# Performance work log

Measured on AMD Instinct MI355X. Metric: run time of the kernel, lower is better.

## Reference

```python
import jax, jax.numpy as jnp
import numpy as np

B, L, D_IN, D_GATE, D_HID, D_STATE = 4, 8192, 512, 2048, 128, 512
EPS = 1e-5


def _layernorm(x, g, b):
    m = jnp.mean(x, axis=-1, keepdims=True)
    v = jnp.var(x, axis=-1, keepdims=True)
    return (x - m) * jax.lax.rsqrt(v + EPS) * g + b


def _dss(u, g, b, lam_re, lam_im, c_re, c_im, d):
    # u: [B, L, H]; diagonal state-space mixing along L via FFT conv
    seq_len = u.shape[-2]
    un = _layernorm(u, g, b)
    residual = un * d                                   # learned skip, [B,L,H]
    lam = -jnp.exp(lam_re) + 1j * jnp.exp(lam_im)       # [N] complex
    c = (c_re + 1j * c_im) * (jnp.exp(lam) - 1.0) / lam  # [H,N]
    t = jnp.arange(seq_len, dtype=jnp.float32)
    s = jnp.exp(t[:, None] * lam[None, :])              # [L,N] Vandermonde
    kern = jnp.einsum('hn,ln->lh', c, s).real           # [L,H]
    n_fft = 2 * seq_len
    uf = jnp.fft.rfft(un, n=n_fft, axis=-2)             # [B, n_fft/2+1, H]
    kf = jnp.fft.rfft(kern, n=n_fft, axis=0)            # [n_fft/2+1, H]
    y = jnp.fft.irfft(uf * kf, n=n_fft, axis=-2)[..., :seq_len, :]
    return y + residual


def setup_inputs() -> dict:
    key = jax.random.key(0)
    ks = jax.random.split(key, 16)
    f32 = jnp.float32
    return {
        'x': jax.random.normal(ks[0], (B, L, D_IN), f32),
        'norm_g': jnp.ones((D_IN,), f32),
        'norm_b': jnp.zeros((D_IN,), f32),
        'W_v': jax.random.normal(ks[1], (D_GATE, D_IN), f32) / np.sqrt(D_IN),
        'W_u': jax.random.normal(ks[2], (D_HID, D_IN), f32) / np.sqrt(D_IN),
        'W_uc': jax.random.normal(ks[3], (D_GATE, D_HID), f32) / np.sqrt(D_HID),
        'W_o': jax.random.normal(ks[4], (D_IN, D_GATE), f32) / np.sqrt(D_GATE),
        'b_o': jnp.zeros((D_IN,), f32),
        'dss_g': jnp.ones((D_HID,), f32),
        'dss_b': jnp.zeros((D_HID,), f32),
        'lam_re': jax.random.normal(ks[5], (D_STATE,), f32),
        'lam_im': jax.random.normal(ks[6], (D_STATE,), f32),
        'C_re': jax.random.normal(ks[7], (D_HID, D_STATE), f32) / np.sqrt(D_STATE),
        'C_im': jax.random.normal(ks[8], (D_HID, D_STATE), f32) / np.sqrt(D_STATE),
        'D_skip': jax.random.normal(ks[9], (D_HID,), f32),
    }


def reference(x, norm_g, norm_b, W_v, W_u, W_uc, W_o, b_o,
              dss_g, dss_b, lam_re, lam_im, C_re, C_im, D_skip):
    xn = _layernorm(x, norm_g, norm_b)
    v = jax.nn.gelu(jnp.einsum('blf,gf->blg', xn, W_v), approximate=False)  # [B,L,G]
    u = jax.nn.gelu(jnp.einsum('blf,hf->blh', xn, W_u), approximate=False)  # [B,L,H]
    y = _dss(u, dss_g, dss_b, lam_re, lam_im, C_re, C_im, D_skip)           # [B,L,H]
    uc = jnp.einsum('blh,gh->blg', y, W_uc)                                 # [B,L,G]
    o = jnp.einsum('blg,fg->blf', uc * v, W_o) + b_o                        # [B,L,F]
    return o + x
```

## Files before the change

kernel.cpp:

```cpp
#include <hip/hip_runtime.h>
#include <math.h>
#include <stdint.h>

typedef unsigned short u16;
typedef unsigned int   u32;
typedef short short8 __attribute__((ext_vector_type(8)));
typedef float v4f    __attribute__((ext_vector_type(4)));

#define DEVI static __device__ __forceinline__

struct __align__(8)  U2 { u32 x, y; };
struct __align__(16) U4 { u32 x, y, z, w; };

static const int BB = 4, LL = 8192;
static const int BL = BB * LL;

DEVI float bf2f(u16 u){ u32 v = ((u32)u) << 16; float f; __builtin_memcpy(&f, &v, 4); return f; }
DEVI u16  f2bf(float f){ u32 u; __builtin_memcpy(&u, &f, 4); return (u16)((u + 0x7fffu + ((u >> 16) & 1u)) >> 16); }

DEVI float geluf(float x){
  float z = fabsf(x) * 0.7071067811865475f;
  float t = __builtin_amdgcn_rcpf(1.0f + 0.3275911f * z);
  float p = t * (0.254829592f + t * (-0.284496736f + t * (1.421413741f +
            t * (-1.453152027f + t * 1.061405429f))));
  float e = __builtin_amdgcn_exp2f(z * z * -1.4426950408889634f);
  float er = 1.0f - p * e;
  float s = (x < 0.0f) ? -er : er;
  return 0.5f * x * (1.0f + s);
}

DEVI void ldsload16(const void* g, void* l){
  __builtin_amdgcn_global_load_lds(
      (const __attribute__((address_space(1))) u32*)(uintptr_t)g,
      (__attribute__((address_space(3)))  u32*)(u32)(uintptr_t)l,
      16, 0, 0);
}

__global__ __launch_bounds__(256) void k_cvt4(
    const float* __restrict__ s0, u16* __restrict__ d0, int n0,
    const float* __restrict__ s1, u16* __restrict__ d1, int n1,
    const float* __restrict__ s2, u16* __restrict__ d2, int n2,
    const float* __restrict__ s3, u16* __restrict__ d3, int n3){
  int i = blockIdx.x * 256 + threadIdx.x;
  if (i < n0){ d0[i] = f2bf(s0[i]); return; }
  i -= n0;
  if (i < n1){ d1[i] = f2bf(s1[i]); return; }
  i -= n1;
  if (i < n2){ d2[i] = f2bf(s2[i]); return; }
  i -= n2;
  if (i < n3){ d3[i] = f2bf(s3[i]); }
}

__global__ __launch_bounds__(256) void k_ln1(const float* __restrict__ x, const float* __restrict__ g,
                                             const float* __restrict__ b, u16* __restrict__ xn){
  int row = blockIdx.x, t = threadIdx.x;
  const float2* xr = (const float2*)(x + (int64_t)row * 512);
  float2 p = xr[t];
  float s = p.x + p.y, ss = p.x * p.x + p.y * p.y;
  for (int off = 32; off; off >>= 1){ s += __shfl_down(s, off); ss += __shfl_down(ss, off); }
  __shared__ float red[8];
  int w = t >> 6, lane = t & 63;
  if (!lane){ red[w] = s; red[4 + w] = ss; }
  __syncthreads();
  s  = red[0] + red[1] + red[2] + red[3];
  ss = red[4] + red[5] + red[6] + red[7];
  float m = s * (1.0f / 512.0f), var = ss * (1.0f / 512.0f) - m * m;
  float rs = rsqrtf(var + 1e-5f);
  float2 gv = ((const float2*)g)[t], bv = ((const float2*)b)[t];
  float r0 = (p.x - m) * rs * gv.x + bv.x;
  float r1 = (p.y - m) * rs * gv.y + bv.y;
  ((u32*)(xn + (int64_t)row * 512))[t] = (u32)f2bf(r0) | ((u32)f2bf(r1) << 16);
}

__global__ __launch_bounds__(256) void k_ln2(const u16* __restrict__ u, const float* __restrict__ g,
                                             const float* __restrict__ b, u16* __restrict__ un){
  int row = blockIdx.x * 4 + (threadIdx.x >> 6);
  int lane = threadIdx.x & 63;
  const u32* ur = (const u32*)(u + (int64_t)row * 128);
  u32 pv = ur[lane];
  float a = bf2f((u16)(pv & 0xffff)), c = bf2f((u16)(pv >> 16));
  float s = a + c, ss = a * a + c * c;
  for (int off = 32; off; off >>= 1){ s += __shfl_xor(s, off); ss += __shfl_xor(ss, off); }
  float m = s * (1.0f / 128.0f), var = ss * (1.0f / 128.0f) - m * m;
  float rs = rsqrtf(var + 1e-5f);
  float2 gv = ((const float2*)g)[lane], bv = ((const float2*)b)[lane];
  float r0 = (a - m) * rs * gv.x + bv.x;
  float r1 = (c - m) * rs * gv.y + bv.y;
  ((u32*)(un + (int64_t)row * 128))[lane] = (u32)f2bf(r0) | ((u32)f2bf(r1) << 16);
}

__global__ __launch_bounds__(256) void k_transpose(const u16* __restrict__ un, u16* __restrict__ unT){
  int bc = blockIdx.x >> 3, it = blockIdx.x & 7;
  int b = bc >> 4, cc = bc & 15;
  __shared__ __align__(16) u16 tile[64][128];
  const u16* src = un + ((int64_t)(b * 8192 + cc * 512 + it * 64)) * 128;
  int t = threadIdx.x;
  for (int p = 0; p < 4; p++){
    int id = p * 256 + t; int ri = id >> 4, seg = id & 15;
    *(U4*)&tile[ri][seg * 8] = *(const U4*)(src + (int64_t)ri * 128 + seg * 8);
  }
  __syncthreads();
  u16* dst = unT + ((int64_t)(bc * 128)) * 512 + it * 64;
  for (int p = 0; p < 4; p++){
    int id = p * 256 + t; int h = id >> 3, seg = id & 7;
    U4 pk; u16* pv = (u16*)&pk;
    for (int k2 = 0; k2 < 8; k2++) pv[k2] = tile[seg * 8 + k2][h];
    *(U4*)(dst + (int64_t)h * 512 + seg * 8) = pk;
  }
}

__global__ __launch_bounds__(512) void k_prep(const float* lam_re, const float* lam_im,
    const float* C_re, const float* C_im,
    u16* ZC, u16* PC, u16* VC, u16* ccat, float* cre, float* cim, float* zT){
  int n = blockIdx.x, t = threadIdx.x;
  float lr = -expf(lam_re[n]);
  float li =  expf(lam_im[n]);
  float mag = expf(lr * (float)t), ph = li * (float)t;
  float er = mag * cosf(ph), ei = mag * sinf(ph);
  ZC[(int64_t)n * 512 + (511 - t)]         = f2bf(er);
  ZC[(int64_t)(512 + n) * 512 + (511 - t)] = f2bf(ei);
  VC[(int64_t)t * 1024 + n]       = f2bf(er);
  VC[(int64_t)t * 1024 + 512 + n] = f2bf(-ei);
  float mag2 = expf(lr * (float)(t + 1)), ph2 = li * (float)(t + 1);
  PC[(int64_t)t * 1024 + n]       = f2bf(mag2 * cosf(ph2));
  PC[(int64_t)t * 1024 + 512 + n] = f2bf(-mag2 * sinf(ph2));
  if (t == 0){
    float m5 = expf(lr * 512.0f), p5 = li * 512.0f;
    zT[n] = m5 * cosf(p5); zT[512 + n] = m5 * sinf(p5);
  }
  if (t < 128){
    float e1m = expf(lr);
    float e1r = e1m * cosf(li), e1i = e1m * sinf(li);
    float nr = e1r - 1.0f, ni = e1i;
    float d2 = lr * lr + li * li;
    float qr = (nr * lr + ni * li) / d2, qi = (ni * lr - nr * li) / d2;
    float Cr = C_re[t * 512 + n], Ci = C_im[t * 512 + n];
    float vr = Cr * qr - Ci * qi, vi = Cr * qi + Ci * qr;
    cre[t * 512 + n] = vr; cim[t * 512 + n] = vi;
    ccat[(int64_t)t * 1024 + n] = f2bf(vr); ccat[(int64_t)t * 1024 + 512 + n] = f2bf(vi);
  }
}

__global__ __launch_bounds__(128) void k_kern(const u16* __restrict__ VC,
                                              const u16* __restrict__ ccat,
                                              float* __restrict__ kern){
  __shared__ __align__(16) u16 vrow[1024];
  int d = blockIdx.x, h = threadIdx.x;
  *(U4*)&vrow[h * 8] = *(const U4*)(VC + (int64_t)d * 1024 + h * 8);
  __syncthreads();
  const u16* cr = ccat + (int64_t)h * 1024;
  float s = 0.0f;
  #pragma unroll 4
  for (int k = 0; k < 1024; k += 8){
    short8 a = *(const short8*)&vrow[k];
    short8 b = *(const short8*)(cr + k);
    #pragma unroll
    for (int j = 0; j < 8; j++) s += bf2f((u16)a[j]) * bf2f((u16)b[j]);
  }
  kern[(int64_t)d * 128 + h] = s;
}

__global__ __launch_bounds__(512) void k_rcat(const float* __restrict__ kern, u16* __restrict__ Rcat){
  int h = blockIdx.x >> 7, a = blockIdx.x & 127;
  int kcol = threadIdx.x;
  int d = 3 - (kcol >> 7);
  int delay = d * 128 + a - (kcol & 127);
  float val = (delay >= 0 && delay < 512) ? kern[delay * 128 + h] : 0.0f;
  Rcat[((int64_t)(h * 128 + a)) * 512 + kcol] = f2bf(val);
}

__global__ __launch_bounds__(256) void k_scan(const float* __restrict__ S, const float* __restrict__ cre,
    const float* __restrict__ cim, const float* __restrict__ zT, u16* __restrict__ WT){
  int tid = blockIdx.x * 256 + threadIdx.x;
  int n = tid & 511, bh = tid >> 9, b = bh >> 7, h = bh & 127;
  float cr = cre[h * 512 + n], ci = cim[h * 512 + n];
  float zr = zT[n], zi = zT[512 + n];
  float sR = 0.0f, sI = 0.0f;
  for (int cc = 0; cc < 16; cc++){
    int64_t m = (int64_t)(b * 16 + cc) * 128 + h;
    float wR = cr * sR - ci * sI, wI = cr * sI + ci * sR;
    WT[m * 1024 + n] = f2bf(wR);
    WT[m * 1024 + 512 + n] = f2bf(wI);
    float aR = S[m * 1024 + n], aI = S[m * 1024 + 512 + n];
    float nR = zr * sR - zi * sI + aR;
    sI = zr * sI + zi * sR + aI;
    sR = nR;
  }
}

__global__ __launch_bounds__(512) void k_assemble2(const float* __restrict__ Yloc,
    const float* __restrict__ Ycross, const u16* __restrict__ un,
    const float* __restrict__ Dskip, u16* __restrict__ y){
  __shared__ float tile[128][65];
  int ii = blockIdx.x;
  int t = threadIdx.x;
  int hl = t >> 6;
  int bcl = t & 63;
  #pragma unroll
  for (int p = 0; p < 16; p++){
    int h = p * 8 + hl;
    tile[h][bcl] = Yloc[((int64_t)(h * 512 + ii)) * 64 + bcl];
  }
  __syncthreads();
  int h = t & 127;
  int bcr = t >> 7;
  float dk = Dskip[h];
  #pragma unroll
  for (int p = 0; p < 16; p++){
    int bc = p * 4 + bcr;
    int b = bc >> 4, cc = bc & 15;
    int64_t e = ((int64_t)b * 8192 + cc * 512 + ii) * 128 + h;
    float val = tile[h][bc]
              + Ycross[(int64_t)ii * 8192 + (int64_t)bc * 128 + h]
              + bf2f(un[e]) * dk;
    y[e] = f2bf(val);
  }
}

template<int EPI, bool TRI = false>
__global__ __launch_bounds__(256) void k_gemm(
    const u16* __restrict__ A, int64_t lda, int64_t aZ,
    const u16* __restrict__ B, int64_t ldb, int64_t bZ,
    void* Cp, int64_t ldc, int64_t cZ,
    int K, int Nvalid,
    const u16* aux1, const float* auxf1, const float* auxf2)
{
  __shared__ union __align__(16) SMU { u16 st[2][4096]; float ep[4][1088]; } sm;
  const int tid = threadIdx.x;
  const int lane = tid & 63, w = tid >> 6;
  const int wr = w >> 1, wc = w & 1, q = lane >> 4, c16 = lane & 15;
  const int sRow = lane >> 2, sSeg = lane & 3;
  const int z = blockIdx.z;

  int bx = blockIdx.x, by = blockIdx.y;
  if (!TRI && (gridDim.y & 7) == 0 && gridDim.x > 1){
    u32 idx = by * gridDim.x + bx;
    u32 xcd = idx & 7, s = idx >> 3;
    bx = s % gridDim.x;
    by = (s / gridDim.x) * 8 + xcd;
  }
  const int64_t m0 = (int64_t)by * 128;
  const int64_t n0 = (int64_t)bx * 128;

  const u16* Ab = A + (int64_t)z * aZ;
  const u16* Bp = B + (int64_t)z * bZ;
  int Keff = K;
  if (TRI){
    Ab += 384 - m0;
    Keff = (int)(m0 + 128);
  }

  v4f acc[4][4];
  #pragma unroll
  for (int i = 0; i < 4; i++)
    #pragma unroll
    for (int j = 0; j < 4; j++)
      acc[i][j] = (v4f)0.0f;

  for (int k0 = 0; k0 < Keff; k0 += 32){
    #pragma unroll
    for (int half = 0; half < 2; half++){
      int r0 = (half * 4 + w) * 16;
      int64_t arow = (TRI ? (int64_t)0 : m0) + r0 + sRow;
      ldsload16(Ab + arow * lda + k0 + sSeg * 8, &sm.st[0][r0 * 32]);
      int64_t brow = n0 + r0 + sRow;
      if (brow >= Nvalid) brow = Nvalid - 1;
      ldsload16(Bp + brow * ldb + k0 + sSeg * 8, &sm.st[1][r0 * 32]);
    }
    __syncthreads();
    short8 af[4], bfr[4];
    const u16* aB = &sm.st[0][(wr * 64 + c16) * 32 + q * 8];
    const u16* bB = &sm.st[1][(wc * 64 + c16) * 32 + q * 8];
    #pragma unroll
    for (int i = 0; i < 4; i++) af[i]  = *(const short8*)(aB + i * 512);
    #pragma unroll
    for (int j = 0; j < 4; j++) bfr[j] = *(const short8*)(bB + j * 512);
    #pragma unroll
    for (int i = 0; i < 4; i++)
      #pragma unroll
      for (int j = 0; j < 4; j++)
        acc[i][j] = __builtin_amdgcn_mfma_f32_16x16x32_bf16(af[i], bfr[j], acc[i][j], 0, 0, 0);
    __syncthreads();
  }

  if (EPI == 0){
    float* Cf = (float*)Cp + (int64_t)z * cZ;
    #pragma unroll
    for (int i = 0; i < 4; i++)
      #pragma unroll
      for (int j = 0; j < 4; j++){
        int64_t gr = m0 + wr * 64 + i * 16 + q * 4;
        int64_t gc = n0 + wc * 64 + j * 16 + c16;
        if (gc < Nvalid){
          #pragma unroll
          for (int r = 0; r < 4; r++)
            Cf[(gr + r) * ldc + gc] = acc[i][j][r];
        }
      }
    return;
  }

  u16* Cb = (u16*)Cp + (int64_t)z * cZ;
  float* ep = sm.ep[w];
  for (int i = 0; i < 4; i++){
    #pragma unroll
    for (int j = 0; j < 4; j++)
      #pragma unroll
      for (int r = 0; r < 4; r++){
        float vv = acc[i][j][r];
        if (EPI == 1) vv = geluf(vv);
        ep[(q * 4 + r) * 68 + j * 16 + c16] = vv;
      }
    #pragma unroll
    for (int p = 0; p < 4; p++){
      int id = p * 64 + lane;
      int row = id >> 4, cg = id & 15;
      float o0 = ep[row * 68 + cg * 4 + 0];
      float o1 = ep[row * 68 + cg * 4 + 1];
      float o2 = ep[row * 68 + cg * 4 + 2];
      float o3 = ep[row * 68 + cg * 4 + 3];
      int64_t gr = m0 + wr * 64 + i * 16 + row;
      int64_t gc = n0 + wc * 64 + cg * 4;
      if (gc < Nvalid){
        U2 outp;
        outp.x = (u32)f2bf(o0) | ((u32)f2bf(o1) << 16);
        outp.y = (u32)f2bf(o2) | ((u32)f2bf(o3) << 16);
        *(U2*)(Cb + gr * ldc + gc) = outp;
      }
    }
  }
}

#define FENCE __builtin_amdgcn_sched_barrier(0)
#define BARX  __builtin_amdgcn_s_barrier()

#define STAGE32(SRC, LD, BUFO, OPO, SEL, KT)                                    \
  { const u16* _g = (SRC) + (int64_t)(KT) * 32 + (int64_t)((SEL) * 128 + wid * 16) * (LD); \
    u16* _lb = smd + (BUFO) + (OPO) + ((SEL) * 128 + wid * 16) * 32;            \
    ldsload16(_g, _lb); }

#define DO_T(T, CUR, FUT)                                                       \
  {                                                                             \
    if ((T) + 2 < NT){                                                          \
      STAGE32(Asrc, lda, (FUT), 0,    0, (T) + 2);                              \
      STAGE32(Asrc, lda, (FUT), 0,    1, (T) + 2);                              \
      STAGE32(Bsrc, ldb, (FUT), 8192, 0, (T) + 2);                              \
      STAGE32(Bsrc, ldb, (FUT), 8192, 1, (T) + 2);                              \
    }                                                                           \
    const char* Ac = (const char*)(smd + (CUR));                                \
    const char* Bc = (const char*)(smd + (CUR) + 8192);                         \
    _Pragma("unroll")                                                           \
    for (int mi = 0; mi < 8; mi++)                                              \
      af[mi] = *(const short8*)(Ac + abase + mi * 1024 + kx);                   \
    _Pragma("unroll")                                                           \
    for (int ni = 0; ni < 4; ni++)                                              \
      bf[ni] = *(const short8*)(Bc + bbase + ni * 1024 + kx);                   \
    __builtin_amdgcn_s_setprio(1);                                              \
    _Pragma("unroll")                                                           \
    for (int mi = 0; mi < 8; mi++)                                              \
      _Pragma("unroll")                                                         \
      for (int ni = 0; ni < 4; ni++)                                            \
        acc[mi][ni] = __builtin_amdgcn_mfma_f32_16x16x32_bf16(                  \
            af[mi], bf[ni], acc[mi][ni], 0, 0, 0);                              \
    __builtin_amdgcn_s_setprio(0);                                              \
    asm volatile("s_waitcnt lgkmcnt(0)" ::: "memory");                          \
    if ((T) + 2 < NT) asm volatile("s_waitcnt vmcnt(4)" ::: "memory");          \
    else              asm volatile("s_waitcnt vmcnt(0)" ::: "memory");          \
    FENCE; BARX; FENCE;                                                         \
  }

template<int EPI>
__global__ __launch_bounds__(512) void k_gemm256(
    const u16* __restrict__ A, int64_t lda,
    const u16* __restrict__ B, int64_t ldb,
    void* __restrict__ Cp, int64_t ldc, int K,
    const u16* __restrict__ aux1,
    const float* __restrict__ auxf1, const float* __restrict__ auxf2)
{
  extern __shared__ __align__(16) u16 smd[];
  const int tid = threadIdx.x, wid = tid >> 6, lane = tid & 63;
  const int wr = wid >> 2, wc = wid & 3, c16 = lane & 15;
  const int q4 = (lane >> 4) << 2;

  int bx = blockIdx.x, by = blockIdx.y;
  if ((gridDim.y & 7) == 0 && gridDim.x > 1){
    u32 idx = by * gridDim.x + bx;
    u32 xcd = idx & 7, s = idx >> 3;
    bx = s % gridDim.x;
    by = (s / gridDim.x) * 8 + xcd;
  }
  const int64_t m0 = (int64_t)by * 256;
  const int64_t n0 = (int64_t)bx * 256;
  const int NT = K >> 5;

  const int rowin = lane >> 2;
  const int chnk  = (lane & 3) ^ ((rowin >> 1) & 3);
  const int colel = chnk * 8;
  const u16* Asrc = A + (m0 + rowin) * lda + colel;
  const u16* Bsrc = B + (n0 + rowin) * ldb + colel;

  const int kx = (((lane >> 4) ^ ((c16 >> 1) & 3)) << 4);
  const int abase = (wr * 128 + c16) * 64;
  const int bbase = (wc * 64 + c16) * 64;

  v4f acc[8][4];
  #pragma unroll
  for (int i = 0; i < 8; i++)
    #pragma unroll
    for (int j = 0; j < 4; j++) acc[i][j] = (v4f)0.0f;

  short8 af[8], bf[4];

  STAGE32(Asrc, lda, 0, 0,    0, 0);
  STAGE32(Asrc, lda, 0, 0,    1, 0);
  STAGE32(Bsrc, ldb, 0, 8192, 0, 0);
  STAGE32(Bsrc, ldb, 0, 8192, 1, 0);
  if (NT > 1){
    STAGE32(Asrc, lda, 16384, 0,    0, 1);
    STAGE32(Asrc, lda, 16384, 0,    1, 1);
    STAGE32(Bsrc, ldb, 16384, 8192, 0, 1);
    STAGE32(Bsrc, ldb, 16384, 8192, 1, 1);
    asm volatile("s_waitcnt vmcnt(4)" ::: "memory");
  } else {
    asm volatile("s_waitcnt vmcnt(0)" ::: "memory");
  }
  FENCE; BARX; FENCE;

  int cur = 0, nxt = 16384, fut = 32768;
  for (int t = 0; t < NT; ++t){
    DO_T(t, cur, fut)
    int tmp = cur; cur = nxt; nxt = fut; fut = tmp;
  }

  if (EPI == 0){
    float* C = (float*)Cp;
    #pragma unroll
    for (int mi = 0; mi < 8; mi++){
      int64_t gr = m0 + wr * 128 + mi * 16 + q4;
      #pragma unroll
      for (int ni = 0; ni < 4; ni++){
        int64_t gc = n0 + wc * 64 + ni * 16 + c16;
        v4f a = acc[mi][ni];
        float bo = auxf2[gc];
        #pragma unroll
        for (int r = 0; r < 4; r++)
          C[(gr + r) * ldc + gc] = a[r] + auxf1[(gr + r) * ldc + gc] + bo;
      }
    }
    return;
  }

  u16* Cb = (u16*)Cp;
  float* scr = (float*)smd + wid * 528;
  const int erow = lane >> 2, eseg = lane & 3;
  #pragma unroll
  for (int mi = 0; mi < 8; mi++){
    #pragma unroll
    for (int nh = 0; nh < 2; nh++){
      #pragma unroll
      for (int ni = 0; ni < 2; ni++){
        v4f a = acc[mi][nh * 2 + ni];
        #pragma unroll
        for (int r = 0; r < 4; r++){
          float vv = a[r];
          if (EPI == 1) vv = geluf(vv);
          scr[(q4 + r) * 33 + ni * 16 + c16] = vv;
        }
      }
      float o[8];
      #pragma unroll
      for (int kq = 0; kq < 8; kq++) o[kq] = scr[erow * 33 + eseg * 8 + kq];
      int64_t gr = m0 + wr * 128 + mi * 16 + erow;
      int64_t gc = n0 + wc * 64 + nh * 32 + eseg * 8;
      if (EPI == 2){
        U4 pv = *(const U4*)(aux1 + gr * ldc + gc);
        const u16* pp = (const u16*)&pv;
        #pragma unroll
        for (int kq = 0; kq < 8; kq++) o[kq] *= bf2f(pp[kq]);
      }
      U4 outp; u16* op = (u16*)&outp;
      #pragma unroll
      for (int kq = 0; kq < 8; kq++) op[kq] = f2bf(o[kq]);
      *(U4*)(Cb + gr * ldc + gc) = outp;
    }
  }
}

extern "C" void kernel_launch(void* const* d_in, const int* in_sizes, int n_in,
                              void* d_out, int out_size, void* d_ws, size_t ws_size,
                              hipStream_t stream) {
  (void)in_sizes; (void)n_in; (void)out_size; (void)ws_size;
  const float* x      = (const float*)d_in[0];
  const float* norm_g = (const float*)d_in[1];
  const float* norm_b = (const float*)d_in[2];
  const float* W_v    = (const float*)d_in[3];
  const float* W_u    = (const float*)d_in[4];
  const float* W_uc   = (const float*)d_in[5];
  const float* W_o    = (const float*)d_in[6];
  const float* b_o    = (const float*)d_in[7];
  const float* dss_g  = (const float*)d_in[8];
  const float* dss_b  = (const float*)d_in[9];
  const float* lam_re = (const float*)d_in[10];
  const float* lam_im = (const float*)d_in[11];
  const float* C_re   = (const float*)d_in[12];
  const float* C_im   = (const float*)d_in[13];
  const float* D_skip = (const float*)d_in[14];

  char* ob = (char*)d_out;
  u16* xn    = (u16*)(ob);
  u16* Wv_b  = (u16*)(ob + 33554432ull);
  u16* Wu_b  = (u16*)(ob + 35651584ull);

  char* ws = (char*)d_ws;
  const size_t R1      = 134217728ull;
  const size_t OFF_UN  = R1 + 33554432ull;
  const size_t OFF_UNT = OFF_UN + 8388608ull;
  const size_t OFF_R2  = OFF_UNT + 8388608ull;
  const size_t OFF_TAB = OFF_R2 + 33554432ull;

  u16*  v     = (u16*)(ws + 0);
  u16*  u     = (u16*)(ws + R1);
  u16*  Rcat  = (u16*)(ws + R1);
  u16*  WT    = (u16*)(ws + R1 + 16777216ull);
  u16*  un    = (u16*)(ws + OFF_UN);
  u16*  unT   = (u16*)(ws + OFF_UNT);
  u16*  y     = (u16*)(ws + OFF_UNT);
  float* S    = (float*)(ws + OFF_R2);
  float* Ycross = (float*)(ws + OFF_R2);
  float* Yloc = (float*)(ws + OFF_R2 + 16777216ull);
  char* tp = ws + OFF_TAB;
  u16*  ZC   = (u16*)tp;            tp += 1048576;
  u16*  PC   = (u16*)tp;            tp += 1048576;
  u16*  VC   = (u16*)tp;            tp += 1048576;
  u16*  ccat = (u16*)tp;            tp += 262144;
  float* cre = (float*)tp;          tp += 262144;
  float* cim = (float*)tp;          tp += 262144;
  float* zT  = (float*)tp;          tp += 4096;
  float* kern= (float*)tp;          tp += 262144;
  u16*  Wo_b = (u16*)tp;            tp += 2097152;
  u16*  Wuc_b= (u16*)tp;            tp += 524288;

  k_cvt4<<<9472, 256, 0, stream>>>(W_v, Wv_b, 2048 * 512,
                                   W_u, Wu_b, 128 * 512,
                                   W_uc, Wuc_b, 2048 * 128,
                                   W_o, Wo_b, 512 * 2048);

  k_ln1<<<BL, 256, 0, stream>>>(x, norm_g, norm_b, xn);
  k_prep<<<512, 512, 0, stream>>>(lam_re, lam_im, C_re, C_im, ZC, PC, VC, ccat, cre, cim, zT);
  k_kern<<<512, 128, 0, stream>>>(VC, ccat, kern);

  k_gemm256<1><<<dim3(8, 128), 512, 98304, stream>>>(xn, 512, Wv_b, 512, v, 2048, 512, nullptr, nullptr, nullptr);
  k_gemm<1><<<dim3(1, 256, 1), 256, 0, stream>>>(xn, 512, 0, Wu_b, 512, 0, u, 128, 0, 512, 128, nullptr, nullptr, nullptr);
  k_ln2<<<BL / 4, 256, 0, stream>>>(u, dss_g, dss_b, un);
  k_transpose<<<512, 256, 0, stream>>>(un, unT);

  k_rcat<<<16384, 512, 0, stream>>>(kern, Rcat);

  k_gemm<0><<<dim3(8, 64, 1), 256, 0, stream>>>(unT, 512, 0, ZC, 512, 0, S, 1024, 0, 512, 1024, nullptr, nullptr, nullptr);
  k_scan<<<1024, 256, 0, stream>>>(S, cre, cim, zT, WT);
  k_gemm<0><<<dim3(64, 4, 1), 256, 0, stream>>>(PC, 1024, 0, WT, 1024, 0, Ycross, 8192, 0, 1024, 8192, nullptr, nullptr, nullptr);
  k_gemm<0, true><<<dim3(1, 4, 128), 256, 0, stream>>>(
      Rcat, 512, 65536, unT, 65536, 512, Yloc, 64, 32768, 512, 64, nullptr, nullptr, nullptr);
  k_assemble2<<<512, 512, 0, stream>>>(Yloc, Ycross, un, D_skip, y);

  k_gemm256<2><<<dim3(8, 128), 512, 98304, stream>>>(y, 128, Wuc_b, 128, v, 2048, 128, v, nullptr, nullptr);
  k_gemm256<0><<<dim3(2, 128), 512, 98304, stream>>>(v, 2048, Wo_b, 2048, d_out, 512, 2048, nullptr, x, b_o);
}
```

Before: 604.4 us.

## Fuse gate GEMM with uc GEMM to avoid v round-trip

Replaces the separate xn·W_v GEMM (with GELU epilogue) and the y·W_uc GEMM (multiplied by v) with one kernel. Each 256x128 tile computes the gate accumulators, applies GELU in registers, then computes the uc accumulators and writes the product once. This removes writing the bf16 v tensor and reading it back. In exchange the tile is narrower (128 columns, twice as many blocks), register pressure rises from holding two accumulator sets, and the smaller K for the uc part pipelines poorly.

```diff
diff --git a/kernel.cpp b/kernel.cpp
--- a/kernel.cpp
+++ b/kernel.cpp
@@ -486,6 +486,169 @@
   }
 }
 
+#define STAGEF(SRC, LD, TBASE, SEL, KT)                                         \
+  { const u16* _g = (SRC) + (int64_t)(KT) * 64 + (int64_t)((SEL) * 128 + wid * 8) * (LD); \
+    u16* _lb = (TBASE) + ((SEL) * 128 + wid * 8) * 64;                          \
+    ldsload16(_g, _lb);                                                         \
+    ldsload16(_g + (int64_t)64 * (LD), _lb + 64 * 64);                          \
+  }
+
+#define CFT(CURB, ACC)                                                          \
+  {                                                                             \
+    const char* Ac = (const char*)(CURB);                                       \
+    const char* Bc = (const char*)(CURB) + 32768;                               \
+    _Pragma("unroll")                                                           \
+    for (int ni = 0; ni < 2; ni++){                                             \
+      bfq[ni][0] = *(const short8*)(Bc + bbase + ni * 2048 + kx0);              \
+      bfq[ni][1] = *(const short8*)(Bc + bbase + ni * 2048 + kx1);              \
+    }                                                                           \
+    _Pragma("unroll")                                                           \
+    for (int mi = 0; mi < 4; mi++){                                             \
+      af[mi][0] = *(const short8*)(Ac + abase + mi * 2048 + kx0);               \
+      af[mi][1] = *(const short8*)(Ac + abase + mi * 2048 + kx1);               \
+    }                                                                           \
+    __builtin_amdgcn_s_setprio(1);                                              \
+    _Pragma("unroll")                                                           \
+    for (int mi = 0; mi < 4; mi++)                                              \
+      _Pragma("unroll")                                                         \
+      for (int ni = 0; ni < 2; ni++){                                           \
+        ACC[mi][ni] = __builtin_amdgcn_mfma_f32_16x16x32_bf16(                  \
+            af[mi][0], bfq[ni][0], ACC[mi][ni], 0, 0, 0);                       \
+        ACC[mi][ni] = __builtin_amdgcn_mfma_f32_16x16x32_bf16(                  \
+            af[mi][1], bfq[ni][1], ACC[mi][ni], 0, 0, 0);                       \
+      }                                                                         \
+    __builtin_amdgcn_s_setprio(0);                                              \
+    _Pragma("unroll")                                                           \
+    for (int mi = 0; mi < 4; mi++){                                             \
+      af[mi][0] = *(const short8*)(Ac + 8192 + abase + mi * 2048 + kx0);        \
+      af[mi][1] = *(const short8*)(Ac + 8192 + abase + mi * 2048 + kx1);        \
+    }                                                                           \
+    __builtin_amdgcn_s_setprio(1);                                              \
+    _Pragma("unroll")                                                           \
+    for (int mi = 0; mi < 4; mi++)                                              \
+      _Pragma("unroll")                                                         \
+      for (int ni = 0; ni < 2; ni++){                                           \
+        ACC[4 + mi][ni] = __builtin_amdgcn_mfma_f32_16x16x32_bf16(              \
+            af[mi][0], bfq[ni][0], ACC[4 + mi][ni], 0, 0, 0);                   \
+        ACC[4 + mi][ni] = __builtin_amdgcn_mfma_f32_16x16x32_bf16(              \
+            af[mi][1], bfq[ni][1], ACC[4 + mi][ni], 0, 0, 0);                   \
+      }                                                                         \
+    __builtin_amdgcn_s_setprio(0);                                              \
+  }
+
+#define DO_FT(T_, NT_, CURB, NXTB, ASRC, ALD, BSRC, BLD, ACC)                   \
+  {                                                                             \
+    if ((T_) + 1 < (NT_)){                                                      \
+      STAGEF(ASRC, ALD, (NXTB),         0, (T_) + 1);                           \
+      STAGEF(ASRC, ALD, (NXTB),         1, (T_) + 1);                           \
+      STAGEF(BSRC, BLD, (NXTB) + 16384, 0, (T_) + 1);                           \
+    }                                                                           \
+    CFT(CURB, ACC)                                                              \
+    asm volatile("s_waitcnt lgkmcnt(0)" ::: "memory");                          \
+    if ((T_) + 1 < (NT_)) asm volatile("s_waitcnt vmcnt(0)" ::: "memory");      \
+    FENCE; BARX; FENCE;                                                         \
+  }
+
+__global__ __launch_bounds__(512) void k_fused(
+    const u16* __restrict__ xn,
+    const u16* __restrict__ Wv,
+    const u16* __restrict__ yb,
+    const u16* __restrict__ Wuc,
+    u16* __restrict__ T)
+{
+  extern __shared__ __align__(16) u16 smd[];
+  const int tid = threadIdx.x, wid = tid >> 6, lane = tid & 63;
+  const int wr = wid >> 2, wc = wid & 3, c16 = lane & 15;
+  const int q4 = (lane >> 4) << 2;
+
+  int bx = blockIdx.x, by = blockIdx.y;
+  if ((gridDim.y & 7) == 0 && gridDim.x > 1){
+    u32 idx = by * gridDim.x + bx;
+    u32 xcd = idx & 7, s = idx >> 3;
+    bx = s % gridDim.x;
+    by = (s / gridDim.x) * 8 + xcd;
+  }
+  const int64_t m0 = (int64_t)by * 256;
+  const int64_t n0 = (int64_t)bx * 128;
+
+  const int rowin = lane >> 3;
+  const int colel = 8 * ((lane & 7) ^ rowin);
+  const u16* Av = xn  + (m0 + rowin) * 512 + colel;
+  const u16* Bv = Wv  + (n0 + rowin) * 512 + colel;
+  const u16* Au = yb  + (m0 + rowin) * 128 + colel;
+  const u16* Bu = Wuc + (n0 + rowin) * 128 + colel;
+
+  const int kx0 = ((lane >> 4) << 4) ^ ((lane & 7) << 4);
+  const int kx1 = kx0 ^ 64;
+  const int abase = (wr * 128 + c16) * 128;
+  const int bbase = (wc * 32 + c16) * 128;
+
+  u16* buf0 = smd;
+  u16* buf1 = smd + 24576;
+
+  v4f accV[8][2], accU[8][2];
+  #pragma unroll
+  for (int i = 0; i < 8; i++)
+    #pragma unroll
+    for (int j = 0; j < 2; j++){ accV[i][j] = (v4f)0.0f; accU[i][j] = (v4f)0.0f; }
+
+  short8 af[4][2], bfq[2][2];
+
+  STAGEF(Av, 512, buf0,         0, 0);
+  STAGEF(Av, 512, buf0,         1, 0);
+  STAGEF(Bv, 512, buf0 + 16384, 0, 0);
+  asm volatile("s_waitcnt vmcnt(0)" ::: "memory");
+  FENCE; BARX; FENCE;
+  for (int t = 0; t < 8; t += 2){
+    DO_FT(t,     8, buf0, buf1, Av, 512, Bv, 512, accV)
+    DO_FT(t + 1, 8, buf1, buf0, Av, 512, Bv, 512, accV)
+  }
+
+  STAGEF(Au, 128, buf0,         0, 0);
+  STAGEF(Au, 128, buf0,         1, 0);
+  STAGEF(Bu, 128, buf0 + 16384, 0, 0);
+  STAGEF(Au, 128, buf1,         0, 1);
+  STAGEF(Au, 128, buf1,         1, 1);
+  STAGEF(Bu, 128, buf1 + 16384, 0, 1);
+  #pragma unroll
+  for (int i = 0; i < 8; i++)
+    #pragma unroll
+    for (int j = 0; j < 2; j++)
+      #pragma unroll
+      for (int r = 0; r < 4; r++)
+        accV[i][j][r] = geluf(accV[i][j][r]);
+  asm volatile("s_waitcnt vmcnt(6)" ::: "memory");
+  FENCE; BARX; FENCE;
+
+  CFT(buf0, accU)
+  asm volatile("s_waitcnt lgkmcnt(0)" ::: "memory");
+  asm volatile("s_waitcnt vmcnt(0)" ::: "memory");
+  FENCE; BARX; FENCE;
+  CFT(buf1, accU)
+
+  float* scr = (float*)smd + wid * 528;
+  const int erow = lane >> 2, eseg = lane & 3;
+  #pragma unroll
+  for (int mi = 0; mi < 8; mi++){
+    #pragma unroll
+    for (int ni = 0; ni < 2; ni++){
+      v4f u = accU[mi][ni], g = accV[mi][ni];
+      #pragma unroll
+      for (int r = 0; r < 4; r++)
+        scr[(q4 + r) * 33 + ni * 16 + c16] = u[r] * g[r];
+    }
+    float o[8];
+    #pragma unroll
+    for (int kq = 0; kq < 8; kq++) o[kq] = scr[erow * 33 + eseg * 8 + kq];
+    int64_t gr = m0 + wr * 128 + mi * 16 + erow;
+    int64_t gc = n0 + wc * 32 + eseg * 8;
+    U4 outp; u16* op = (u16*)&outp;
+    #pragma unroll
+    for (int kq = 0; kq < 8; kq++) op[kq] = f2bf(o[kq]);
+    *(U4*)(T + gr * 2048 + gc) = outp;
+  }
+}
+
 extern "C" void kernel_launch(void* const* d_in, const int* in_sizes, int n_in,
                               void* d_out, int out_size, void* d_ws, size_t ws_size,
                               hipStream_t stream) {
@@ -549,7 +712,6 @@
   k_prep<<<512, 512, 0, stream>>>(lam_re, lam_im, C_re, C_im, ZC, PC, VC, ccat, cre, cim, zT);
   k_kern<<<512, 128, 0, stream>>>(VC, ccat, kern);
 
-  k_gemm256<1><<<dim3(8, 128), 512, 98304, stream>>>(xn, 512, Wv_b, 512, v, 2048, 512, nullptr, nullptr, nullptr);
   k_gemm<1><<<dim3(1, 256, 1), 256, 0, stream>>>(xn, 512, 0, Wu_b, 512, 0, u, 128, 0, 512, 128, nullptr, nullptr, nullptr);
   k_ln2<<<BL / 4, 256, 0, stream>>>(u, dss_g, dss_b, un);
   k_transpose<<<512, 256, 0, stream>>>(un, unT);
@@ -563,6 +725,6 @@
       Rcat, 512, 65536, unT, 65536, 512, Yloc, 64, 32768, 512, 64, nullptr, nullptr, nullptr);
   k_assemble2<<<512, 512, 0, stream>>>(Yloc, Ycross, un, D_skip, y);
 
-  k_gemm256<2><<<dim3(8, 128), 512, 98304, stream>>>(y, 128, Wuc_b, 128, v, 2048, 128, v, nullptr, nullptr);
+  k_fused<<<dim3(16, 128), 512, 98304, stream>>>(xn, Wv_b, y, Wuc_b, v);
   k_gemm256<0><<<dim3(2, 128), 512, 98304, stream>>>(v, 2048, Wo_b, 2048, d_out, 512, 2048, nullptr, x, b_o);
 }
```

After: 553.3 us. -8.4%, faster.
